# Kernel tuning notes

Measured on AMD Instinct MI355X. Metric: run time of the kernel, lower is better.

Reference implementation:

```python
import jax, jax.numpy as jnp
import numpy as np

V, D, E, N, Dd, Dc, NL, B, L = 50280, 1024, 2048, 16, 64, 4, 2, 2, 1024
EPS = 1e-5


def rmsnorm(x, w):
    return x * jax.lax.rsqrt(jnp.mean(x * x, axis=-1, keepdims=True) + EPS) * w


def setup_inputs() -> dict:
    key = jax.random.key(0)
    ks = jax.random.split(key, 18)
    n = jax.random.normal
    inp = {
        "input_ids": jax.random.randint(ks[0], (B, L), 0, V),
        "embedding": n(ks[1], (V, D), jnp.float32) * 0.02,
        "lm_head_w": n(ks[2], (V, D), jnp.float32) * 0.02,
        "norm_w": jnp.ones((D,), jnp.float32),
        # stacked per-layer params (leading dim = n_layer)
        "l_norm_w": jnp.ones((NL, D), jnp.float32),
        "l_skip_w": n(ks[3], (NL, E, D), jnp.float32) / np.sqrt(D),
        "l_in_w": n(ks[4], (NL, E, D), jnp.float32) / np.sqrt(D),
        "l_conv_w": n(ks[5], (NL, E, 1, Dc), jnp.float32) / np.sqrt(Dc),
        "l_conv_b": jnp.zeros((NL, E), jnp.float32),
        "l_Wd1": n(ks[6], (NL, Dd, E), jnp.float32) / np.sqrt(E),
        "l_Wd2_w": n(ks[7], (NL, E, Dd), jnp.float32) / np.sqrt(Dd),
        "l_Wd2_b": n(ks[8], (NL, E), jnp.float32) * 0.1 - 4.0,  # small dt init
        "l_WB": n(ks[9], (NL, N, E), jnp.float32) / np.sqrt(E),
        "l_WC": n(ks[10], (NL, N, E), jnp.float32) / np.sqrt(E),
        "l_A_log": jnp.log(jax.random.uniform(ks[11], (NL, E, N), jnp.float32, 0.5, 1.2)),
        "l_WD": jnp.ones((NL, E), jnp.float32),
        "l_out_w": n(ks[12], (NL, D, E), jnp.float32) / np.sqrt(E),
    }
    return inp


def mamba_layer(resid, norm_w, skip_w, in_w, conv_w, conv_b, Wd1, Wd2_w, Wd2_b,
                WB, WC, A_log, WD, out_w):
    x = rmsnorm(resid, norm_w)                      # [B,L,D]
    skip = x @ skip_w.T                             # [B,L,E]
    x = x @ in_w.T                                  # [B,L,E]
    # depthwise causal conv (pad D_conv-1 on left == pad both + slice [:L])
    xc = jax.lax.conv_general_dilated(
        x.transpose(0, 2, 1), conv_w, (1,), [(Dc - 1, 0)],
        feature_group_count=E, dimension_numbers=("NCH", "OIH", "NCH"))
    x = (xc + conv_b[None, :, None]).transpose(0, 2, 1)  # [B,L,E]
    x = jax.nn.silu(x)

    delta = jax.nn.softplus((x @ Wd1.T) @ Wd2_w.T + Wd2_b)  # [B,L,E]
    A = -jnp.exp(A_log)                                      # [E,N]
    A_bar = jnp.exp(delta[..., None] * A)                    # [B,L,E,N]
    Bt = x @ WB.T                                            # [B,L,N]
    Ct = x @ WC.T                                            # [B,L,N]
    Bx = (delta * x)[..., None] * Bt[:, :, None, :]          # [B,L,E,N]

    def step(h, inp):
        Ab_t, Bx_t, C_t = inp                                # [B,E,N],[B,E,N],[B,N]
        h = Ab_t * h + Bx_t
        y = jnp.einsum("ben,bn->be", h, C_t)
        return h, y

    h0 = jnp.zeros((B, E, N), x.dtype)
    _, ys = jax.lax.scan(step, h0,
                         (A_bar.transpose(1, 0, 2, 3), Bx.transpose(1, 0, 2, 3),
                          Ct.transpose(1, 0, 2)))
    y = ys.transpose(1, 0, 2)                                # [B,L,E]
    y = y + x * WD
    y = y * jax.nn.silu(skip)
    return resid + y @ out_w.T


def reference(input_ids, embedding, lm_head_w, norm_w, l_norm_w, l_skip_w, l_in_w,
              l_conv_w, l_conv_b, l_Wd1, l_Wd2_w, l_Wd2_b, l_WB, l_WC, l_A_log,
              l_WD, l_out_w):
    resid = embedding[input_ids]                             # [B,L,D]
    for i in range(NL):
        resid = mamba_layer(resid, l_norm_w[i], l_skip_w[i], l_in_w[i],
                            l_conv_w[i], l_conv_b[i], l_Wd1[i], l_Wd2_w[i],
                            l_Wd2_b[i], l_WB[i], l_WC[i], l_A_log[i], l_WD[i],
                            l_out_w[i])
    resid = rmsnorm(resid, norm_w)
    return resid @ lm_head_w.T                               # [B,L,V]
```

## Files before the change

### kernel.cpp

```cpp
#include <hip/hip_runtime.h>

typedef unsigned short u16;
using bf16x8 = __attribute__((ext_vector_type(8))) __bf16;
using f32x4  = __attribute__((ext_vector_type(4))) float;

typedef const void __attribute__((address_space(1))) gvoid_t;
typedef void __attribute__((address_space(3))) lvoid_t;

#define NL 2
#define Bd 2
#define Ld 1024
#define Dd_ 1024
#define Ed 2048
#define Nd 16
#define TOK (Bd*Ld)
#define VPAD 50432
#define VREAL 50280
#define NCHUNK 16
#define CLEN 64
#define XLD 4096

__device__ __forceinline__ u16 f2bf(float f) {
    union { float f; unsigned u; } v; v.f = f;
    unsigned u = v.u;
    unsigned r = (u + 0x7fffu + ((u >> 16) & 1u)) >> 16;
    return (u16)r;
}
__device__ __forceinline__ float bf2f(u16 u) {
    union { unsigned u; float f; } v; v.u = ((unsigned)u) << 16; return v.f;
}
__device__ __forceinline__ unsigned pk2(float a, float b) {
    return (unsigned)f2bf(a) | ((unsigned)f2bf(b) << 16);
}
__device__ __forceinline__ float siluf(float x) { return x / (1.f + __expf(-x)); }
__device__ __forceinline__ float softplusf(float z) {
    return (z > 15.f) ? z : log1pf(__expf(z));
}

__global__ void k_convert_all(const float* __restrict__ lmw, const float* __restrict__ lskip,
                              const float* __restrict__ linw, const float* __restrict__ loutw,
                              const float* __restrict__ lWd2, const float* __restrict__ lWd1,
                              const float* __restrict__ lWB, const float* __restrict__ lWC,
                              u16* __restrict__ lm_bf, u16* __restrict__ wsi_bf,
                              u16* __restrict__ wout_bf, u16* __restrict__ wd2_bf,
                              u16* __restrict__ wsml_bf) {
    int g = blockIdx.x * 256 + threadIdx.x;
    const float* src = nullptr; u16* dst = nullptr;
    if (g < 6455296) {
        dst = lm_bf + (size_t)g * 8;
        if (g < 6435840) src = lmw + (size_t)g * 8;
    } else if (g < 7503872) {
        int i = g - 6455296;
        int layer = i >> 19;
        int within = i & 524287;
        int mat = within >> 18;
        int idx = within & 262143;
        src = (mat ? linw : lskip) + ((size_t)layer << 21) + ((size_t)idx * 8);
        dst = wsi_bf + ((size_t)layer << 22) + ((size_t)mat << 21) + ((size_t)idx * 8);
    } else if (g < 8028160) {
        int i = g - 7503872;
        src = loutw + (size_t)i * 8; dst = wout_bf + (size_t)i * 8;
    } else if (g < 8060928) {
        int i = g - 8028160;
        src = lWd2 + (size_t)i * 8; dst = wd2_bf + (size_t)i * 8;
    } else {
        int i = g - 8060928;
        int layer = i >> 15;
        int j = i & 32767;
        int col = (j * 8) & 2047;
        int r = (j * 8) >> 11;
        const float* s2 = nullptr;
        if (r < 64) s2 = lWd1 + ((size_t)layer * 64 + r) * 2048;
        else if (r < 80) s2 = lWB + ((size_t)layer * 16 + (r - 64)) * 2048;
        else if (r < 96) s2 = lWC + ((size_t)layer * 16 + (r - 80)) * 2048;
        dst = wsml_bf + ((size_t)layer << 18) + (size_t)j * 8;
        if (s2) src = s2 + col;
    }
    uint4 o;
    if (src) {
        float4 v0 = *(const float4*)src;
        float4 v1 = *(const float4*)(src + 4);
        o.x = pk2(v0.x, v0.y); o.y = pk2(v0.z, v0.w);
        o.z = pk2(v1.x, v1.y); o.w = pk2(v1.z, v1.w);
    } else { o.x = o.y = o.z = o.w = 0; }
    *(uint4*)dst = o;
}

__global__ void k_embed_norm(const int* __restrict__ ids, const float* __restrict__ emb,
                             const float* __restrict__ w, float* __restrict__ resid,
                             u16* __restrict__ out) {
    int tk = blockIdx.x, tid = threadIdx.x;
    int id = ids[tk];
    float4 v = *(const float4*)&emb[(size_t)id * Dd_ + tid * 4];
    *(float4*)&resid[(size_t)tk * Dd_ + tid * 4] = v;
    float ss = v.x * v.x + v.y * v.y + v.z * v.z + v.w * v.w;
    #pragma unroll
    for (int m = 32; m; m >>= 1) ss += __shfl_xor(ss, m);
    __shared__ float red[4];
    if ((tid & 63) == 0) red[tid >> 6] = ss;
    __syncthreads();
    ss = red[0] + red[1] + red[2] + red[3];
    float rs = rsqrtf(ss * (1.f / 1024.f) + 1e-5f);
    float4 wv = *(const float4*)&w[tid * 4];
    ushort4 o;
    o.x = f2bf(v.x * rs * wv.x); o.y = f2bf(v.y * rs * wv.y);
    o.z = f2bf(v.z * rs * wv.z); o.w = f2bf(v.w * rs * wv.w);
    *(ushort4*)&out[(size_t)tk * Dd_ + tid * 4] = o;
}

__global__ void k_add2_norm(const float* __restrict__ part, float* __restrict__ resid,
                            const float* __restrict__ w, u16* __restrict__ out) {
    int tk = blockIdx.x, tid = threadIdx.x;
    size_t i4 = (size_t)tk * Dd_ + tid * 4;
    float4 r = *(const float4*)&resid[i4];
    float4 a = *(const float4*)&part[i4];
    float4 b = *(const float4*)&part[(size_t)TOK * Dd_ + i4];
    r.x += a.x + b.x; r.y += a.y + b.y; r.z += a.z + b.z; r.w += a.w + b.w;
    *(float4*)&resid[i4] = r;
    float ss = r.x * r.x + r.y * r.y + r.z * r.z + r.w * r.w;
    #pragma unroll
    for (int m = 32; m; m >>= 1) ss += __shfl_xor(ss, m);
    __shared__ float red[4];
    if ((tid & 63) == 0) red[tid >> 6] = ss;
    __syncthreads();
    ss = red[0] + red[1] + red[2] + red[3];
    float rs = rsqrtf(ss * (1.f / 1024.f) + 1e-5f);
    float4 wv = *(const float4*)&w[tid * 4];
    ushort4 o;
    o.x = f2bf(r.x * rs * wv.x); o.y = f2bf(r.y * rs * wv.y);
    o.z = f2bf(r.z * rs * wv.z); o.w = f2bf(r.w * rs * wv.w);
    *(ushort4*)&out[(size_t)tk * Dd_ + tid * 4] = o;
}

__global__ void k_conv_silu(const u16* __restrict__ xin, const float* __restrict__ cw,
                            const float* __restrict__ cb, u16* __restrict__ xbf) {
    int blk = blockIdx.x;
    int tk = blk >> 1;
    int e0 = ((blk & 1) << 10) + threadIdx.x * 4;
    int b = tk >> 10, l = tk & 1023;
    float4 w0 = *(const float4*)&cw[(size_t)(e0 + 0) * 4];
    float4 w1 = *(const float4*)&cw[(size_t)(e0 + 1) * 4];
    float4 w2 = *(const float4*)&cw[(size_t)(e0 + 2) * 4];
    float4 w3 = *(const float4*)&cw[(size_t)(e0 + 3) * 4];
    float4 bv = *(const float4*)&cb[e0];
    float a0 = bv.x, a1 = bv.y, a2 = bv.z, a3 = bv.w;
    const float* wp0 = (const float*)&w0; const float* wp1 = (const float*)&w1;
    const float* wp2 = (const float*)&w2; const float* wp3 = (const float*)&w3;
    #pragma unroll
    for (int k = 0; k < 4; ++k) {
        int ll = l - 3 + k;
        if (ll < 0) continue;
        ushort4 xv = *(const ushort4*)&xin[((size_t)(b * 1024 + ll)) * XLD + e0];
        a0 = fmaf(bf2f(xv.x), wp0[k], a0); a1 = fmaf(bf2f(xv.y), wp1[k], a1);
        a2 = fmaf(bf2f(xv.z), wp2[k], a2); a3 = fmaf(bf2f(xv.w), wp3[k], a3);
    }
    a0 = siluf(a0); a1 = siluf(a1); a2 = siluf(a2); a3 = siluf(a3);
    ushort4 ob; ob.x = f2bf(a0); ob.y = f2bf(a1); ob.z = f2bf(a2); ob.w = f2bf(a3);
    *(ushort4*)&xbf[(size_t)tk * Ed + e0] = ob;
}

__global__ void k_reduce_xs(const float* __restrict__ part, float* __restrict__ xs,
                            u16* __restrict__ xsbf) {
    size_t i4 = ((size_t)blockIdx.x * 256 + threadIdx.x) * 4;
    float4 s = *(const float4*)&part[i4];
    #pragma unroll
    for (int c = 1; c < 8; ++c) {
        float4 v = *(const float4*)&part[(size_t)c * TOK * 128 + i4];
        s.x += v.x; s.y += v.y; s.z += v.z; s.w += v.w;
    }
    *(float4*)&xs[i4] = s;
    ushort4 o; o.x = f2bf(s.x); o.y = f2bf(s.y); o.z = f2bf(s.z); o.w = f2bf(s.w);
    *(ushort4*)&xsbf[i4] = o;
}

__global__ void k_scan_pass1(const float* __restrict__ delta, const u16* __restrict__ x,
                             const float* __restrict__ xs, const float* __restrict__ A_log,
                             float* __restrict__ sumd, float* __restrict__ Hc) {
    __shared__ float sBt[CLEN][16];
    int t = blockIdx.x * 256 + threadIdx.x;
    int e = t & (Ed - 1);
    int cb = t >> 11;
    int b = cb & 1, c = cb >> 1;
    int rowbase = b * 1024 + c * CLEN;
    {
        int f = threadIdx.x * 4;
        int row = f >> 4, cc = f & 15;
        float4 v = *(const float4*)&xs[(size_t)(rowbase + row) * 128 + 64 + cc];
        *(float4*)&sBt[row][cc] = v;
    }
    __syncthreads();
    float dA[16], h[16];
    #pragma unroll
    for (int n = 0; n < 16; ++n) { dA[n] = -__expf(A_log[e * 16 + n]); h[n] = 0.f; }
    float sd = 0.f;
    for (int l = 0; l < CLEN; ++l) {
        size_t row = (size_t)rowbase + l;
        float dlt = delta[row * Ed + e];
        float xv  = bf2f(x[row * Ed + e]);
        sd += dlt;
        float dx = dlt * xv;
        float4 bt0 = *(const float4*)&sBt[l][0];
        float4 bt1 = *(const float4*)&sBt[l][4];
        float4 bt2 = *(const float4*)&sBt[l][8];
        float4 bt3 = *(const float4*)&sBt[l][12];
        float bts[16] = {bt0.x,bt0.y,bt0.z,bt0.w, bt1.x,bt1.y,bt1.z,bt1.w,
                         bt2.x,bt2.y,bt2.z,bt2.w, bt3.x,bt3.y,bt3.z,bt3.w};
        #pragma unroll
        for (int n = 0; n < 16; ++n) {
            float a = __expf(dA[n] * dlt);
            h[n] = fmaf(a, h[n], dx * bts[n]);
        }
    }
    size_t gg = (size_t)cb * Ed + e;
    #pragma unroll
    for (int n = 0; n < 16; ++n) Hc[gg * 16 + n] = h[n];
    sumd[gg] = sd;
}

__global__ void k_scan_pass2(const float* __restrict__ delta, const u16* __restrict__ x,
                             const float* __restrict__ xs, const float* __restrict__ A_log,
                             const float* __restrict__ sumd, const float* __restrict__ Hc,
                             const float* __restrict__ WD,
                             const u16* __restrict__ skipg, u16* __restrict__ ybf) {
    __shared__ float sBC[CLEN][32];
    int t = blockIdx.x * 256 + threadIdx.x;
    int e = t & (Ed - 1);
    int cb = t >> 11;
    int b = cb & 1, c = cb >> 1;
    int rowbase = b * 1024 + c * CLEN;
    {
        int f = threadIdx.x * 8;
        int row = f >> 5, cc = f & 31;
        float4 v0 = *(const float4*)&xs[(size_t)(rowbase + row) * 128 + 64 + cc];
        float4 v1 = *(const float4*)&xs[(size_t)(rowbase + row) * 128 + 64 + cc + 4];
        *(float4*)&sBC[row][cc] = v0;
        *(float4*)&sBC[row][cc + 4] = v1;
    }
    __syncthreads();
    float dA[16], h[16];
    #pragma unroll
    for (int n = 0; n < 16; ++n) {
        dA[n] = -__expf(A_log[e * 16 + n]);
        h[n] = 0.f;
    }
    for (int cc = 0; cc < c; ++cc) {
        size_t g2 = ((size_t)(cc * Bd + b) * Ed + e);
        float sdc = sumd[g2];
        #pragma unroll
        for (int n = 0; n < 16; ++n)
            h[n] = fmaf(__expf(dA[n] * sdc), h[n], Hc[g2 * 16 + n]);
    }
    float wd = WD[e];
    for (int l = 0; l < CLEN; ++l) {
        size_t row = (size_t)rowbase + l;
        float dlt = delta[row * Ed + e];
        float xv  = bf2f(x[row * Ed + e]);
        float dx = dlt * xv;
        float4 b0 = *(const float4*)&sBC[l][0];
        float4 b1 = *(const float4*)&sBC[l][4];
        float4 b2 = *(const float4*)&sBC[l][8];
        float4 b3 = *(const float4*)&sBC[l][12];
        float4 c0 = *(const float4*)&sBC[l][16];
        float4 c1 = *(const float4*)&sBC[l][20];
        float4 c2 = *(const float4*)&sBC[l][24];
        float4 c3 = *(const float4*)&sBC[l][28];
        float bts[16] = {b0.x,b0.y,b0.z,b0.w, b1.x,b1.y,b1.z,b1.w,
                         b2.x,b2.y,b2.z,b2.w, b3.x,b3.y,b3.z,b3.w};
        float cts[16] = {c0.x,c0.y,c0.z,c0.w, c1.x,c1.y,c1.z,c1.w,
                         c2.x,c2.y,c2.z,c2.w, c3.x,c3.y,c3.z,c3.w};
        float y = 0.f;
        #pragma unroll
        for (int n = 0; n < 16; ++n) {
            float a = __expf(dA[n] * dlt);
            h[n] = fmaf(a, h[n], dx * bts[n]);
            y = fmaf(h[n], cts[n], y);
        }
        float yo = y + xv * wd;
        float sk = bf2f(skipg[row * XLD + e]);
        ybf[row * Ed + e] = f2bf(yo * siluf(sk));
    }
}

template<int EPI>
__global__ __launch_bounds__(256, 2)
void k_gemm_bt(const u16* __restrict__ A, int lda,
               const u16* __restrict__ B, int ldb,
               float* __restrict__ C, int ldc,
               const float* __restrict__ aux,
               int ntm, int Nstore, int Kc, size_t Cz) {
    __shared__ u16 lsA[2][128 * 32];
    __shared__ u16 lsB[2][128 * 32];
    int kz = blockIdx.z;
    A += (size_t)kz * Kc;
    B += (size_t)kz * Kc;
    C += (size_t)kz * Cz;
    int tid = threadIdx.x;
    int bid = blockIdx.x;
    int mt = bid % ntm, nt = bid / ntm;
    int mBase = mt * 128, nBase = nt * 128;
    int lane = tid & 63, wid = tid >> 6;
    int wr = wid >> 1, wc = wid & 1;

    f32x4 acc[4][4] = {};
    const u16* Ablk = A + (size_t)mBase * lda;
    const u16* Bblk = B + (size_t)nBase * ldb;
    int nk = Kc >> 5;

    auto stage = [&](int buf, int kt) {
        #pragma unroll
        for (int i = 0; i < 2; ++i) {
            int chunk = i * 256 + tid;
            int row = chunk >> 2;
            int kc  = (chunk & 3) << 3;
            const u16* ga = Ablk + (size_t)row * lda + (kt << 5) + kc;
            const u16* gb = Bblk + (size_t)row * ldb + (kt << 5) + kc;
            u16* la = &lsA[buf][(size_t)(i * 256 + wid * 64) * 8];
            u16* lb = &lsB[buf][(size_t)(i * 256 + wid * 64) * 8];
            __builtin_amdgcn_global_load_lds((gvoid_t*)ga, (lvoid_t*)la, 16, 0, 0);
            __builtin_amdgcn_global_load_lds((gvoid_t*)gb, (lvoid_t*)lb, 16, 0, 0);
        }
    };
    auto compute = [&](int buf) {
        bf16x8 af[4], bfr[4];
        const u16* baseA = lsA[buf];
        const u16* baseB = lsB[buf];
        int kq = (lane >> 4) << 3;
        int r  = lane & 15;
        #pragma unroll
        for (int mi = 0; mi < 4; ++mi)
            af[mi] = *(const bf16x8*)&baseA[(size_t)((wr * 64 + mi * 16 + r) * 32 + kq)];
        #pragma unroll
        for (int ni = 0; ni < 4; ++ni)
            bfr[ni] = *(const bf16x8*)&baseB[(size_t)((wc * 64 + ni * 16 + r) * 32 + kq)];
        #pragma unroll
        for (int mi = 0; mi < 4; ++mi)
            #pragma unroll
            for (int ni = 0; ni < 4; ++ni)
                acc[mi][ni] = __builtin_amdgcn_mfma_f32_16x16x32_bf16(af[mi], bfr[ni], acc[mi][ni], 0, 0, 0);
    };

    stage(0, 0);
    asm volatile("s_waitcnt vmcnt(0)" ::: "memory");
    __syncthreads();
    int cur = 0;
    for (int kt = 0; kt + 1 < nk; ++kt) {
        stage(cur ^ 1, kt + 1);
        compute(cur);
        asm volatile("s_waitcnt vmcnt(0)" ::: "memory");
        __syncthreads();
        cur ^= 1;
    }
    compute(cur);

    int rbase = (lane >> 4) * 4, ccol = lane & 15;
    #pragma unroll
    for (int mi = 0; mi < 4; ++mi) {
        #pragma unroll
        for (int ni = 0; ni < 4; ++ni) {
            int gc = nBase + wc * 64 + ni * 16 + ccol;
            if (gc < Nstore) {
                float bias = (EPI == 2) ? aux[gc] : 0.f;
                #pragma unroll
                for (int rr = 0; rr < 4; ++rr) {
                    int gr = mBase + wr * 64 + mi * 16 + rbase + rr;
                    size_t off = (size_t)gr * ldc + gc;
                    float v = acc[mi][ni][rr];
                    if (EPI == 2) v = softplusf(v + bias);
                    if (EPI == 3) ((u16*)C)[off] = f2bf(v);
                    else          C[off] = v;
                }
            }
        }
    }
}

#define BAR()    asm volatile("s_barrier" ::: "memory")
#define WAITV2() asm volatile("s_waitcnt vmcnt(2)" ::: "memory")
#define WAITV0() asm volatile("s_waitcnt vmcnt(0)" ::: "memory")

#define STG(buf, mat, h, kt) { \
    const u16* _s0 = ((mat) ? srcB[(h)*2]     : srcA[(h)*2])     + (size_t)(kt) * 64; \
    const u16* _s1 = ((mat) ? srcB[(h)*2 + 1] : srcA[(h)*2 + 1]) + (size_t)(kt) * 64; \
    char* _d = (char*)&ls[buf][mat][0]; \
    __builtin_amdgcn_global_load_lds((gvoid_t*)_s0, (lvoid_t*)(_d + (h)*16384 + tid*16), 16, 0, 0); \
    __builtin_amdgcn_global_load_lds((gvoid_t*)_s1, (lvoid_t*)(_d + (h)*16384 + 8192 + tid*16), 16, 0, 0); }

#define QUAD(buf, kk, mih) { \
    const char* _pa = (const char*)&ls[buf][0][0]; \
    const char* _pb = (const char*)&ls[buf][1][0]; \
    bf16x8 _af[4], _bf[4]; \
    _Pragma("unroll") \
    for (int _m = 0; _m < 4; ++_m) \
        _af[_m] = *(const bf16x8*)(_pa + abase + ((mih)*4 + _m) * 2048 + (kk) * 1024); \
    _Pragma("unroll") \
    for (int _n = 0; _n < 4; ++_n) \
        _bf[_n] = *(const bf16x8*)(_pb + bbase + _n * 2048 + (kk) * 1024); \
    __builtin_amdgcn_s_setprio(1); \
    _Pragma("unroll") \
    for (int _m = 0; _m < 4; ++_m) \
        _Pragma("unroll") \
        for (int _n = 0; _n < 4; ++_n) \
            acc[(mih)*4 + _m][_n] = __builtin_amdgcn_mfma_f32_16x16x32_bf16(_af[_m], _bf[_n], acc[(mih)*4 + _m][_n], 0, 0, 0); \
    __builtin_amdgcn_s_setprio(0); }

__global__ __launch_bounds__(512, 2)
void k_gemm256(const u16* __restrict__ A, int lda,
               const u16* __restrict__ B, int ldb,
               float* __restrict__ C, int ldc,
               int ntm, int Nstore, int K) {
    __shared__ u16 ls[2][2][256 * 64];
    const int tid = threadIdx.x;
    const int lane = tid & 63, wid = tid >> 6;
    const int wr = wid >> 2, wc = wid & 3;

    int nwg = gridDim.x, bid = blockIdx.x;
    int q8 = nwg >> 3, r8 = nwg & 7;
    int xcd = bid & 7, linb = bid >> 3;
    int sb = (xcd < r8 ? xcd * (q8 + 1) : r8 * (q8 + 1) + (xcd - r8) * q8) + linb;
    int mt = sb % ntm, nt = sb / ntm;

    const u16* Ablk = A + (size_t)(mt * 256) * lda;
    const u16* Bblk = B + (size_t)(nt * 256) * ldb;

    const u16* srcA[4]; const u16* srcB[4];
    #pragma unroll
    for (int s = 0; s < 4; ++s) {
        int p = s * 8192 + tid * 16;
        int qq = p ^ (((p >> 9) & 1) << 5);
        int sub = qq >> 10, rin = (qq >> 6) & 15, cby = qq & 63;
        int row = ((sub >> 1) << 4) | rin;
        int col = ((((sub & 1) << 6) | cby)) >> 1;
        srcA[s] = Ablk + (size_t)row * lda + col;
        srcB[s] = Bblk + (size_t)row * ldb + col;
    }
    int l15 = lane & 15;
    int lowb = (l15 * 64 + ((lane >> 4) << 4)) ^ (((l15 >> 3) & 1) << 5);
    int abase = wr * 16384 + lowb;
    int bbase = wc * 8192  + lowb;

    f32x4 acc[8][4] = {};
    int nk = K >> 6, nit = nk >> 1;

    STG(0, 0, 0, 0); STG(0, 0, 1, 0); STG(0, 1, 0, 0); STG(0, 1, 1, 0);

    for (int i = 0; i < nit; ++i) {
        int t1 = 2 * i + 1, t2 = 2 * i + 2;
        bool more = (i + 1 < nit);
        STG(1, 0, 0, t1);
        WAITV2(); BAR();
        QUAD(0, 0, 0); BAR();
        STG(1, 0, 1, t1);
        QUAD(0, 0, 1); BAR();
        STG(1, 1, 0, t1);
        QUAD(0, 1, 0); BAR();
        STG(1, 1, 1, t1);
        QUAD(0, 1, 1); BAR();
        if (more) { STG(0, 0, 0, t2); WAITV2(); } else { WAITV0(); }
        BAR();
        QUAD(1, 0, 0); BAR();
        if (more) STG(0, 0, 1, t2);
        QUAD(1, 0, 1); BAR();
        if (more) STG(0, 1, 0, t2);
        QUAD(1, 1, 0); BAR();
        if (more) STG(0, 1, 1, t2);
        QUAD(1, 1, 1); BAR();
    }

    int rb = (lane >> 4) * 4, cc = lane & 15;
    int mrow = mt * 256 + wr * 128, ncol = nt * 256 + wc * 64;
    #pragma unroll
    for (int mi = 0; mi < 8; ++mi) {
        #pragma unroll
        for (int ni = 0; ni < 4; ++ni) {
            int gc = ncol + ni * 16 + cc;
            if (gc < Nstore) {
                #pragma unroll
                for (int rr = 0; rr < 4; ++rr) {
                    size_t off = (size_t)(mrow + mi * 16 + rb + rr) * ldc + gc;
                    C[off] = acc[mi][ni][rr];
                }
            }
        }
    }
}

extern "C" void kernel_launch(void* const* d_in, const int* in_sizes, int n_in,
                              void* d_out, int out_size, void* d_ws, size_t ws_size,
                              hipStream_t stream) {
    const int*   ids   = (const int*)d_in[0];
    const float* emb   = (const float*)d_in[1];
    const float* lmw   = (const float*)d_in[2];
    const float* normw = (const float*)d_in[3];
    const float* lnw   = (const float*)d_in[4];
    const float* lskip = (const float*)d_in[5];
    const float* linw  = (const float*)d_in[6];
    const float* lcw   = (const float*)d_in[7];
    const float* lcb   = (const float*)d_in[8];
    const float* lWd1  = (const float*)d_in[9];
    const float* lWd2  = (const float*)d_in[10];
    const float* lWd2b = (const float*)d_in[11];
    const float* lWB   = (const float*)d_in[12];
    const float* lWC   = (const float*)d_in[13];
    const float* lAlog = (const float*)d_in[14];
    const float* lWD   = (const float*)d_in[15];
    const float* loutw = (const float*)d_in[16];
    float* out = (float*)d_out;

    char* ws = (char*)d_ws;
    size_t off = 0;
    auto alloc = [&](size_t bytes) { char* p = ws + off; off += (bytes + 255) & ~(size_t)255; return p; };
    u16*   lm_bf    = (u16*)  alloc((size_t)VPAD * 1024 * 2);
    u16*   wsi_bf   = (u16*)  alloc((size_t)NL * 4096 * Dd_ * 2);
    u16*   wout_bf  = (u16*)  alloc((size_t)NL * Dd_ * Ed * 2);
    u16*   wd2_bf   = (u16*)  alloc((size_t)NL * Ed * 64 * 2);
    u16*   wsml_bf  = (u16*)  alloc((size_t)NL * 128 * Ed * 2);
    float* resid    = (float*)alloc((size_t)TOK * Dd_ * 4);
    u16*   xn_bf    = (u16*)  alloc((size_t)TOK * Dd_ * 2);
    u16*   xall_bf  = (u16*)  alloc((size_t)TOK * XLD * 2);
    u16*   xbf      = (u16*)  alloc((size_t)TOK * Ed * 2);
    float* xs       = (float*)alloc((size_t)TOK * 128 * 4);
    u16*   xs_bf    = (u16*)  alloc((size_t)TOK * 128 * 2);
    float* xs_part  = (float*)alloc((size_t)8 * TOK * 128 * 4);
    float* opart    = (float*)alloc((size_t)2 * TOK * Dd_ * 4);
    float* delta    = (float*)alloc((size_t)TOK * Ed * 4);
    float* sumd     = (float*)alloc((size_t)NCHUNK * Bd * Ed * 4);
    float* Hc       = (float*)alloc((size_t)NCHUNK * Bd * Ed * Nd * 4);
    u16*   ybf      = (u16*)  alloc((size_t)TOK * Ed * 2);
    (void)ws_size; (void)in_sizes; (void)n_in; (void)out_size;

    k_convert_all<<<31744, 256, 0, stream>>>(lmw, lskip, linw, loutw, lWd2, lWd1, lWB, lWC,
                                             lm_bf, wsi_bf, wout_bf, wd2_bf, wsml_bf);

    k_embed_norm<<<TOK, 256, 0, stream>>>(ids, emb, lnw, resid, xn_bf);

    for (int lyr = 0; lyr < NL; ++lyr) {
        const float* Alog = lAlog + (size_t)lyr * Ed * Nd;
        k_gemm_bt<3><<<dim3(16 * 32, 1, 1), 256, 0, stream>>>(xn_bf, Dd_,
            wsi_bf + (size_t)lyr * 4096 * Dd_, Dd_, (float*)xall_bf, XLD, nullptr,
            16, 4096, 1024, 0);
        k_conv_silu<<<TOK * 2, 256, 0, stream>>>(xall_bf + Ed, lcw + (size_t)lyr * Ed * 4,
                                                 lcb + (size_t)lyr * Ed, xbf);
        k_gemm_bt<0><<<dim3(16, 1, 8), 256, 0, stream>>>(xbf, Ed,
            wsml_bf + (size_t)lyr * 128 * Ed, Ed, xs_part, 128, nullptr, 16, 128, 256,
            (size_t)TOK * 128);
        k_reduce_xs<<<TOK * 128 / 4 / 256, 256, 0, stream>>>(xs_part, xs, xs_bf);
        k_gemm_bt<2><<<dim3(16 * 16, 1, 1), 256, 0, stream>>>(xs_bf, 128,
            wd2_bf + (size_t)lyr * Ed * 64, 64, delta, Ed, lWd2b + (size_t)lyr * Ed,
            16, Ed, 64, 0);
        k_scan_pass1<<<NCHUNK * Bd * Ed / 256, 256, 0, stream>>>(delta, xbf, xs, Alog, sumd, Hc);
        k_scan_pass2<<<NCHUNK * Bd * Ed / 256, 256, 0, stream>>>(delta, xbf, xs, Alog,
            sumd, Hc, lWD + (size_t)lyr * Ed, xall_bf, ybf);
        k_gemm_bt<0><<<dim3(16 * 8, 1, 2), 256, 0, stream>>>(ybf, Ed,
            wout_bf + (size_t)lyr * Dd_ * Ed, Ed, opart, Dd_, nullptr, 16, Dd_, 1024,
            (size_t)TOK * Dd_);
        const float* nw = (lyr == NL - 1) ? normw : lnw + (size_t)(lyr + 1) * Dd_;
        k_add2_norm<<<TOK, 256, 0, stream>>>(opart, resid, nw, xn_bf);
    }

    k_gemm256<<<dim3(8 * (VPAD / 256), 1, 1), 512, 0, stream>>>(xn_bf, Dd_, lm_bf, Dd_,
        out, VREAL, 8, VREAL, 1024);
}
```

Baseline: 784.6 us.

## Store delta and out-proj partials in bf16, use 256-tile GEMM for in-proj

The delta tensor and the split-K out-projection partial sums are now written as bf16 instead of fp32, with a new epilogue mode for softplus plus bf16 store. The scan kernels and the add-norm kernel read them back as bf16. This halves the memory traffic for these intermediates. The in-projection GEMM also moves from the 128-tile kernel to the larger 256-tile kernel, which is templated to emit bf16. The trade-off is lower precision for delta and the residual update.

```diff
diff --git a/kernel.cpp b/kernel.cpp
--- a/kernel.cpp
+++ b/kernel.cpp
@@ -108,14 +108,15 @@
     *(ushort4*)&out[(size_t)tk * Dd_ + tid * 4] = o;
 }
 
-__global__ void k_add2_norm(const float* __restrict__ part, float* __restrict__ resid,
+__global__ void k_add2_norm(const u16* __restrict__ part, float* __restrict__ resid,
                             const float* __restrict__ w, u16* __restrict__ out) {
     int tk = blockIdx.x, tid = threadIdx.x;
     size_t i4 = (size_t)tk * Dd_ + tid * 4;
     float4 r = *(const float4*)&resid[i4];
-    float4 a = *(const float4*)&part[i4];
-    float4 b = *(const float4*)&part[(size_t)TOK * Dd_ + i4];
-    r.x += a.x + b.x; r.y += a.y + b.y; r.z += a.z + b.z; r.w += a.w + b.w;
+    ushort4 a = *(const ushort4*)&part[i4];
+    ushort4 b = *(const ushort4*)&part[(size_t)TOK * Dd_ + i4];
+    r.x += bf2f(a.x) + bf2f(b.x); r.y += bf2f(a.y) + bf2f(b.y);
+    r.z += bf2f(a.z) + bf2f(b.z); r.w += bf2f(a.w) + bf2f(b.w);
     *(float4*)&resid[i4] = r;
     float ss = r.x * r.x + r.y * r.y + r.z * r.z + r.w * r.w;
     #pragma unroll
@@ -173,7 +174,7 @@
     *(ushort4*)&xsbf[i4] = o;
 }
 
-__global__ void k_scan_pass1(const float* __restrict__ delta, const u16* __restrict__ x,
+__global__ void k_scan_pass1(const u16* __restrict__ delta, const u16* __restrict__ x,
                              const float* __restrict__ xs, const float* __restrict__ A_log,
                              float* __restrict__ sumd, float* __restrict__ Hc) {
     __shared__ float sBt[CLEN][16];
@@ -195,7 +196,7 @@
     float sd = 0.f;
     for (int l = 0; l < CLEN; ++l) {
         size_t row = (size_t)rowbase + l;
-        float dlt = delta[row * Ed + e];
+        float dlt = bf2f(delta[row * Ed + e]);
         float xv  = bf2f(x[row * Ed + e]);
         sd += dlt;
         float dx = dlt * xv;
@@ -217,7 +218,7 @@
     sumd[gg] = sd;
 }
 
-__global__ void k_scan_pass2(const float* __restrict__ delta, const u16* __restrict__ x,
+__global__ void k_scan_pass2(const u16* __restrict__ delta, const u16* __restrict__ x,
                              const float* __restrict__ xs, const float* __restrict__ A_log,
                              const float* __restrict__ sumd, const float* __restrict__ Hc,
                              const float* __restrict__ WD,
@@ -253,7 +254,7 @@
     float wd = WD[e];
     for (int l = 0; l < CLEN; ++l) {
         size_t row = (size_t)rowbase + l;
-        float dlt = delta[row * Ed + e];
+        float dlt = bf2f(delta[row * Ed + e]);
         float xv  = bf2f(x[row * Ed + e]);
         float dx = dlt * xv;
         float4 b0 = *(const float4*)&sBC[l][0];
@@ -293,7 +294,8 @@
     int kz = blockIdx.z;
     A += (size_t)kz * Kc;
     B += (size_t)kz * Kc;
-    C += (size_t)kz * Cz;
+    if (EPI == 3 || EPI == 4) C = (float*)((u16*)C + (size_t)kz * Cz);
+    else                      C += (size_t)kz * Cz;
     int tid = threadIdx.x;
     int bid = blockIdx.x;
     int mt = bid % ntm, nt = bid / ntm;
@@ -359,15 +361,15 @@
         for (int ni = 0; ni < 4; ++ni) {
             int gc = nBase + wc * 64 + ni * 16 + ccol;
             if (gc < Nstore) {
-                float bias = (EPI == 2) ? aux[gc] : 0.f;
+                float bias = (EPI == 4) ? aux[gc] : 0.f;
                 #pragma unroll
                 for (int rr = 0; rr < 4; ++rr) {
                     int gr = mBase + wr * 64 + mi * 16 + rbase + rr;
                     size_t off = (size_t)gr * ldc + gc;
                     float v = acc[mi][ni][rr];
-                    if (EPI == 2) v = softplusf(v + bias);
-                    if (EPI == 3) ((u16*)C)[off] = f2bf(v);
-                    else          C[off] = v;
+                    if (EPI == 4) v = softplusf(v + bias);
+                    if (EPI == 3 || EPI == 4) ((u16*)C)[off] = f2bf(v);
+                    else                      C[off] = v;
                 }
             }
         }
@@ -403,6 +405,7 @@
             acc[(mih)*4 + _m][_n] = __builtin_amdgcn_mfma_f32_16x16x32_bf16(_af[_m], _bf[_n], acc[(mih)*4 + _m][_n], 0, 0, 0); \
     __builtin_amdgcn_s_setprio(0); }
 
+template<int EPI>
 __global__ __launch_bounds__(512, 2)
 void k_gemm256(const u16* __restrict__ A, int lda,
                const u16* __restrict__ B, int ldb,
@@ -477,7 +480,8 @@
                 #pragma unroll
                 for (int rr = 0; rr < 4; ++rr) {
                     size_t off = (size_t)(mrow + mi * 16 + rb + rr) * ldc + gc;
-                    C[off] = acc[mi][ni][rr];
+                    if (EPI == 3) ((u16*)C)[off] = f2bf(acc[mi][ni][rr]);
+                    else          C[off] = acc[mi][ni][rr];
                 }
             }
         }
@@ -521,8 +525,8 @@
     float* xs       = (float*)alloc((size_t)TOK * 128 * 4);
     u16*   xs_bf    = (u16*)  alloc((size_t)TOK * 128 * 2);
     float* xs_part  = (float*)alloc((size_t)8 * TOK * 128 * 4);
-    float* opart    = (float*)alloc((size_t)2 * TOK * Dd_ * 4);
-    float* delta    = (float*)alloc((size_t)TOK * Ed * 4);
+    u16*   opart    = (u16*)  alloc((size_t)2 * TOK * Dd_ * 2);
+    u16*   delta    = (u16*)  alloc((size_t)TOK * Ed * 2);
     float* sumd     = (float*)alloc((size_t)NCHUNK * Bd * Ed * 4);
     float* Hc       = (float*)alloc((size_t)NCHUNK * Bd * Ed * Nd * 4);
     u16*   ybf      = (u16*)  alloc((size_t)TOK * Ed * 2);
@@ -535,28 +539,27 @@
 
     for (int lyr = 0; lyr < NL; ++lyr) {
         const float* Alog = lAlog + (size_t)lyr * Ed * Nd;
-        k_gemm_bt<3><<<dim3(16 * 32, 1, 1), 256, 0, stream>>>(xn_bf, Dd_,
-            wsi_bf + (size_t)lyr * 4096 * Dd_, Dd_, (float*)xall_bf, XLD, nullptr,
-            16, 4096, 1024, 0);
+        k_gemm256<3><<<dim3(8 * 16, 1, 1), 512, 0, stream>>>(xn_bf, Dd_,
+            wsi_bf + (size_t)lyr * 4096 * Dd_, Dd_, (float*)xall_bf, XLD, 8, 4096, 1024);
         k_conv_silu<<<TOK * 2, 256, 0, stream>>>(xall_bf + Ed, lcw + (size_t)lyr * Ed * 4,
                                                  lcb + (size_t)lyr * Ed, xbf);
         k_gemm_bt<0><<<dim3(16, 1, 8), 256, 0, stream>>>(xbf, Ed,
             wsml_bf + (size_t)lyr * 128 * Ed, Ed, xs_part, 128, nullptr, 16, 128, 256,
             (size_t)TOK * 128);
         k_reduce_xs<<<TOK * 128 / 4 / 256, 256, 0, stream>>>(xs_part, xs, xs_bf);
-        k_gemm_bt<2><<<dim3(16 * 16, 1, 1), 256, 0, stream>>>(xs_bf, 128,
-            wd2_bf + (size_t)lyr * Ed * 64, 64, delta, Ed, lWd2b + (size_t)lyr * Ed,
+        k_gemm_bt<4><<<dim3(16 * 16, 1, 1), 256, 0, stream>>>(xs_bf, 128,
+            wd2_bf + (size_t)lyr * Ed * 64, 64, (float*)delta, Ed, lWd2b + (size_t)lyr * Ed,
             16, Ed, 64, 0);
         k_scan_pass1<<<NCHUNK * Bd * Ed / 256, 256, 0, stream>>>(delta, xbf, xs, Alog, sumd, Hc);
         k_scan_pass2<<<NCHUNK * Bd * Ed / 256, 256, 0, stream>>>(delta, xbf, xs, Alog,
             sumd, Hc, lWD + (size_t)lyr * Ed, xall_bf, ybf);
-        k_gemm_bt<0><<<dim3(16 * 8, 1, 2), 256, 0, stream>>>(ybf, Ed,
-            wout_bf + (size_t)lyr * Dd_ * Ed, Ed, opart, Dd_, nullptr, 16, Dd_, 1024,
+        k_gemm_bt<3><<<dim3(16 * 8, 1, 2), 256, 0, stream>>>(ybf, Ed,
+            wout_bf + (size_t)lyr * Dd_ * Ed, Ed, (float*)opart, Dd_, nullptr, 16, Dd_, 1024,
             (size_t)TOK * Dd_);
         const float* nw = (lyr == NL - 1) ? normw : lnw + (size_t)(lyr + 1) * Dd_;
         k_add2_norm<<<TOK, 256, 0, stream>>>(opart, resid, nw, xn_bf);
     }
 
-    k_gemm256<<<dim3(8 * (VPAD / 256), 1, 1), 512, 0, stream>>>(xn_bf, Dd_, lm_bf, Dd_,
+    k_gemm256<0><<<dim3(8 * (VPAD / 256), 1, 1), 512, 0, stream>>>(xn_bf, Dd_, lm_bf, Dd_,
         out, VREAL, 8, VREAL, 1024);
 }
```

New measurement: 801.4 us. 2.1% more time.
